# Kernel optimization log

Hardware: AMD Instinct MI355X
Metric: run time of the kernel (lower is better)

Reference implementation:

```python
import jax, jax.numpy as jnp
import numpy as np

B1, B2 = 4096, 4096
DF, MF = 1024, 512
H1, H2, H3, H1_ = 2048, 1024, 512, 1024
DO, MO = 1, 1


def _lin(x, W, b):
    return x @ W.T + b


def setup_inputs() -> dict:
    key = jax.random.key(0)
    ks = jax.random.split(key, 22)

    def w(k, o, i):
        return (jax.random.normal(k, (o, i), jnp.float32) / np.sqrt(i)).astype(jnp.float32)

    def bz(k, o):
        return jax.random.normal(k, (o,), jnp.float32) * 0.01

    return {
        'x1': jax.random.normal(ks[0], (B1, DF), jnp.float32),
        'x2': jax.random.normal(ks[1], (B2, MF), jnp.float32),
        'W1_1': w(ks[2], H1, DF),  'b1_1': bz(ks[3], H1),
        'W1_2': w(ks[4], H2, H1),  'b1_2': bz(ks[5], H2),
        'W1_3': w(ks[6], H3, H2),  'b1_3': bz(ks[7], H3),
        'W1_4': w(ks[8], H2, H3),  'b1_4': bz(ks[9], H2),
        'W1_5': w(ks[10], H1, H2), 'b1_5': bz(ks[11], H1),
        'Wp1':  w(ks[12], DO, H1), 'bp1':  bz(ks[13], DO),
        'W2_1': w(ks[14], H1_, MF), 'b2_1': bz(ks[15], H1_),
        'W2_2': w(ks[16], H3, H1_), 'b2_2': bz(ks[17], H3),
        'W2_3': w(ks[18], H1_, H3), 'b2_3': bz(ks[19], H1_),
        'Wp2':  w(ks[20], MO, H1_), 'bp2':  bz(ks[21], MO),
    }


def reference(x1, x2, W1_1, b1_1, W1_2, b1_2, W1_3, b1_3, W1_4, b1_4,
              W1_5, b1_5, Wp1, bp1, W2_1, b2_1, W2_2, b2_2, W2_3, b2_3,
              Wp2, bp2):
    # dropout: eval mode (identity)
    h = jax.nn.relu(_lin(x1, W1_1, b1_1))
    h = jax.nn.relu(_lin(h, W1_2, b1_2))
    x_1 = jax.nn.sigmoid(_lin(h, W1_3, b1_3))          # [B1, H3]
    h = jax.nn.relu(_lin(x_1, W1_4, b1_4))
    h = jax.nn.relu(_lin(h, W1_5, b1_5))
    x2_1 = jax.nn.sigmoid(_lin(h, Wp1, bp1))           # [B1, DO]

    g = jax.nn.relu(_lin(x2, W2_1, b2_1))
    x_2 = jax.nn.sigmoid(_lin(g, W2_2, b2_2))          # [B2, H3]
    g = jax.nn.relu(_lin(x_2, W2_3, b2_3))
    x2_2 = jax.nn.sigmoid(_lin(g, Wp2, bp2))           # [B2, MO]

    # Python loop over x_1 rows doing (x_2 * row).sum(1) == single GEMM x_1 @ x_2.T
    scores = x_1 @ x_2.T                                # [B1, B2]
    pre_dm = scores.reshape(-1)                         # row-major matches torch.cat order
    # MinMaxScaler.fit_transform on detached values (original uses .data -> no grad)
    pre_dm = jax.lax.stop_gradient(pre_dm)
    mn, mx = pre_dm.min(), pre_dm.max()
    pre_dm = (pre_dm - mn) / (mx - mn)

    pre_data = x2_1.reshape(-1)
    pre_model = x2_2.T.reshape(-1)
    return (pre_data, pre_dm, pre_model)
```

## Files before the change

### kernel.cpp

```cpp
#include <hip/hip_runtime.h>
#include <hip/hip_bf16.h>

typedef __bf16 bf16_t;
typedef bf16_t bf16x8 __attribute__((ext_vector_type(8)));
typedef bf16_t bf16x4 __attribute__((ext_vector_type(4)));
typedef float f32x4 __attribute__((ext_vector_type(4)));

typedef __attribute__((address_space(1))) const void gconst_void;
typedef __attribute__((address_space(3))) void lds_void;

__device__ __forceinline__ void async16(const bf16_t* g, bf16_t* l) {
  __builtin_amdgcn_global_load_lds((gconst_void*)g, (lds_void*)l, 16, 0, 0);
}

struct CvtDesc { const float* src; bf16_t* dst; long n; };
struct CvtArgs { CvtDesc d[10]; };

__global__ __launch_bounds__(256) void cvt_many(CvtArgs a) {
  const CvtDesc de = a.d[blockIdx.y];
  long i = ((long)blockIdx.x * 256 + threadIdx.x) * 4;
  const long stride = (long)gridDim.x * 256 * 4;
  for (; i < de.n; i += stride) {
    float4 v = *(const float4*)(de.src + i);
    bf16x4 o;
    o[0] = (bf16_t)v.x; o[1] = (bf16_t)v.y; o[2] = (bf16_t)v.z; o[3] = (bf16_t)v.w;
    *(bf16x4*)(de.dst + i) = o;
  }
}

struct GDesc {
  const bf16_t* A; const bf16_t* W; const float* bias; void* C;
  int N, K, act;
};
struct GArgs { GDesc d[2]; int ntiles0; };

template <typename OutT, bool MINMAX>
__global__ __launch_bounds__(256) void gemm_gb(GArgs ga, float* __restrict__ pmin,
                                               float* __restrict__ pmax) {
  const int b = blockIdx.x;
  const int p = (b >= ga.ntiles0) ? 1 : 0;
  const GDesc d = ga.d[p];
  const int local = b - (p ? ga.ntiles0 : 0);
  const int bm = (local & 31) * 128;
  const int bn = (local >> 5) * 64;
  const int N = d.N, K = d.K;

  __shared__ __align__(16) bf16_t As[2][128 * 32];
  __shared__ __align__(16) bf16_t Bs[2][64 * 32];

  const int t = threadIdx.x;
  const int wave = t >> 6;
  const int lane = t & 63;
  const int quad = lane >> 4;
  const int l15 = lane & 15;
  const int wm = (wave >> 1) * 64;
  const int wn = (wave & 1) * 32;

  f32x4 acc[4][2];
#pragma unroll
  for (int i = 0; i < 4; ++i)
#pragma unroll
    for (int j = 0; j < 2; ++j) acc[i][j] = (f32x4){0.f, 0.f, 0.f, 0.f};

  const int c0 = t, c1 = t + 256;
  const int r0 = c0 >> 2, kc0 = ((c0 & 3) - r0) & 3;
  const int r1 = c1 >> 2, kc1 = ((c1 & 3) - r1) & 3;
  const bf16_t* pa0 = d.A + (long)(bm + r0) * K + kc0 * 8;
  const bf16_t* pa1 = d.A + (long)(bm + r1) * K + kc1 * 8;
  const bf16_t* pw0 = d.W + (long)(bn + r0) * K + kc0 * 8;
  bf16_t* lA0 = &As[0][c0 * 8]; bf16_t* lA1 = &As[0][c1 * 8];
  bf16_t* lB0 = &Bs[0][c0 * 8];
  const int bufOffA = 128 * 32;
  const int bufOffB = 64 * 32;

  async16(pa0, lA0); async16(pa1, lA1);
  async16(pw0, lB0);

  int buf = 0;
  for (int k0 = 0; k0 < K; k0 += 32) {
    __syncthreads();
    const int kn = k0 + 32;
    if (kn < K) {
      const int oA = (buf ^ 1) * bufOffA;
      const int oB = (buf ^ 1) * bufOffB;
      async16(pa0 + kn, lA0 + oA); async16(pa1 + kn, lA1 + oA);
      async16(pw0 + kn, lB0 + oB);
    }
    const bf16_t* as = As[buf];
    const bf16_t* bs = Bs[buf];
    bf16x8 af[4], bfr[2];
#pragma unroll
    for (int i = 0; i < 4; ++i) {
      const int r = wm + i * 16 + l15;
      af[i] = *(const bf16x8*)&as[r * 32 + ((quad + r) & 3) * 8];
    }
#pragma unroll
    for (int j = 0; j < 2; ++j) {
      const int r = wn + j * 16 + l15;
      bfr[j] = *(const bf16x8*)&bs[r * 32 + ((quad + r) & 3) * 8];
    }
#pragma unroll
    for (int i = 0; i < 4; ++i)
#pragma unroll
      for (int j = 0; j < 2; ++j)
        acc[i][j] = __builtin_amdgcn_mfma_f32_16x16x32_bf16(bfr[j], af[i],
                                                            acc[i][j], 0, 0, 0);
    buf ^= 1;
  }

  OutT* C = (OutT*)d.C;
  const int row0 = bm + wm + l15;
  const int col0 = bn + wn + quad * 4;
  float mn = 3.4e38f, mx = -3.4e38f;
#pragma unroll
  for (int i = 0; i < 4; ++i) {
    const long row = row0 + i * 16;
#pragma unroll
    for (int j = 0; j < 2; ++j) {
      const int col = col0 + j * 16;
      f32x4 bv = d.bias ? *(const f32x4*)&d.bias[col] : (f32x4){0.f, 0.f, 0.f, 0.f};
      f32x4 v;
#pragma unroll
      for (int r = 0; r < 4; ++r) {
        float x = acc[i][j][r] + bv[r];
        if (d.act == 1) x = fmaxf(x, 0.f);
        else if (d.act == 2) x = 1.f / (1.f + expf(-x));
        v[r] = x;
        if (MINMAX) { mn = fminf(mn, x); mx = fmaxf(mx, x); }
      }
      if constexpr (sizeof(OutT) == 4) {
        *(f32x4*)&((float*)C)[row * N + col] = v;
      } else {
        bf16x4 o;
        o[0] = (bf16_t)v[0]; o[1] = (bf16_t)v[1];
        o[2] = (bf16_t)v[2]; o[3] = (bf16_t)v[3];
        *(bf16x4*)&((bf16_t*)C)[row * N + col] = o;
      }
    }
  }
  if (MINMAX) {
#pragma unroll
    for (int off = 32; off > 0; off >>= 1) {
      mn = fminf(mn, __shfl_down(mn, off));
      mx = fmaxf(mx, __shfl_down(mx, off));
    }
    __shared__ float smn[4], smx[4];
    if (lane == 0) { smn[wave] = mn; smx[wave] = mx; }
    __syncthreads();
    if (t == 0) {
      pmin[blockIdx.x] = fminf(fminf(smn[0], smn[1]), fminf(smn[2], smn[3]));
      pmax[blockIdx.x] = fmaxf(fmaxf(smx[0], smx[1]), fmaxf(smx[2], smx[3]));
    }
  }
}

struct RDesc { const bf16_t* A; const float* w; const float* b; float* out; int K; };

__global__ __launch_bounds__(64) void rowdot2(RDesc d0, RDesc d1) {
  const RDesc d = blockIdx.y ? d1 : d0;
  const int row = blockIdx.x;
  const int lane = threadIdx.x;
  const bf16_t* a = d.A + (long)row * d.K;
  float s = 0.f;
  for (int k = lane * 8; k < d.K; k += 64 * 8) {
    bf16x8 av = *(const bf16x8*)&a[k];
    float4 w0 = *(const float4*)&d.w[k];
    float4 w1 = *(const float4*)&d.w[k + 4];
    s += (float)av[0] * w0.x + (float)av[1] * w0.y +
         (float)av[2] * w0.z + (float)av[3] * w0.w +
         (float)av[4] * w1.x + (float)av[5] * w1.y +
         (float)av[6] * w1.z + (float)av[7] * w1.w;
  }
#pragma unroll
  for (int off = 32; off > 0; off >>= 1) s += __shfl_down(s, off);
  if (lane == 0) d.out[row] = 1.f / (1.f + expf(-(s + d.b[0])));
}

__global__ __launch_bounds__(256) void minmax_final(
    const float* __restrict__ pmin, const float* __restrict__ pmax, int nb,
    float* __restrict__ res) {
  float mn = 3.4e38f, mx = -3.4e38f;
  for (int i = threadIdx.x; i < nb; i += 256) {
    mn = fminf(mn, pmin[i]);
    mx = fmaxf(mx, pmax[i]);
  }
#pragma unroll
  for (int off = 32; off > 0; off >>= 1) {
    mn = fminf(mn, __shfl_down(mn, off));
    mx = fmaxf(mx, __shfl_down(mx, off));
  }
  __shared__ float smn[4], smx[4];
  const int wv = threadIdx.x >> 6, ln = threadIdx.x & 63;
  if (ln == 0) { smn[wv] = mn; smx[wv] = mx; }
  __syncthreads();
  if (threadIdx.x == 0) {
    float m0 = fminf(fminf(smn[0], smn[1]), fminf(smn[2], smn[3]));
    float m1 = fmaxf(fmaxf(smx[0], smx[1]), fmaxf(smx[2], smx[3]));
    res[0] = m0;
    res[1] = 1.f / (m1 - m0);
  }
}

__global__ __launch_bounds__(256) void normalize_k(
    float* __restrict__ out, const float* __restrict__ res, long n) {
  const float mn = res[0], inv = res[1];
  long i = ((long)blockIdx.x * 256 + threadIdx.x) * 4;
  const long stride = (long)gridDim.x * 256 * 4;
  for (; i < n; i += stride) {
    float4 v = *(const float4*)&out[i];
    v.x = (v.x - mn) * inv;
    v.y = (v.y - mn) * inv;
    v.z = (v.z - mn) * inv;
    v.w = (v.w - mn) * inv;
    *(float4*)&out[i] = v;
  }
}

extern "C" void kernel_launch(void* const* d_in, const int* in_sizes, int n_in,
                              void* d_out, int out_size, void* d_ws,
                              size_t ws_size, hipStream_t stream) {
  const float* x1   = (const float*)d_in[0];
  const float* x2   = (const float*)d_in[1];
  const float* W1_1 = (const float*)d_in[2];   const float* b1_1 = (const float*)d_in[3];
  const float* W1_2 = (const float*)d_in[4];   const float* b1_2 = (const float*)d_in[5];
  const float* W1_3 = (const float*)d_in[6];   const float* b1_3 = (const float*)d_in[7];
  const float* W1_4 = (const float*)d_in[8];   const float* b1_4 = (const float*)d_in[9];
  const float* W1_5 = (const float*)d_in[10];  const float* b1_5 = (const float*)d_in[11];
  const float* Wp1  = (const float*)d_in[12];  const float* bp1  = (const float*)d_in[13];
  const float* W2_1 = (const float*)d_in[14];  const float* b2_1 = (const float*)d_in[15];
  const float* W2_2 = (const float*)d_in[16];  const float* b2_2 = (const float*)d_in[17];
  const float* W2_3 = (const float*)d_in[18];  const float* b2_3 = (const float*)d_in[19];
  const float* Wp2  = (const float*)d_in[20];  const float* bp2  = (const float*)d_in[21];

  float* out = (float*)d_out;
  float* out_pre_data  = out;
  float* out_pre_dm    = out + 4096;
  float* out_pre_model = out + 4096 + (long)4096 * 4096;

  char* arena = (char*)out_pre_dm;
  const size_t MB = 1024 * 1024;
  bf16_t* x1b   = (bf16_t*)(arena);
  bf16_t* x2b   = (bf16_t*)(arena + 8 * MB);
  bf16_t* W1_1b = (bf16_t*)(arena + 12 * MB);
  bf16_t* W1_2b = (bf16_t*)(arena + 16 * MB);
  bf16_t* W1_3b = (bf16_t*)(arena + 20 * MB);
  bf16_t* W1_4b = (bf16_t*)(arena + 21 * MB);
  bf16_t* W1_5b = (bf16_t*)(arena + 22 * MB);
  bf16_t* W2_1b = (bf16_t*)(arena + 26 * MB);
  bf16_t* W2_2b = (bf16_t*)(arena + 27 * MB);
  bf16_t* W2_3b = (bf16_t*)(arena + 28 * MB);
  bf16_t* bufA  = (bf16_t*)(arena + 32 * MB);
  bf16_t* bufB  = (bf16_t*)(arena + 48 * MB);
  bf16_t* bufC  = (bf16_t*)(arena + 56 * MB);

  char* ws = (char*)d_ws;
  bf16_t* bufX1 = (bf16_t*)(ws);
  bf16_t* bufX2 = (bf16_t*)(ws + 4 * MB);
  float* pmin = (float*)(ws + 8 * MB);
  float* pmax = pmin + 2048;
  float* res  = pmax + 2048;

  CvtArgs ca;
  ca.d[0] = {x1,   x1b,   (long)4096 * 1024};
  ca.d[1] = {x2,   x2b,   (long)4096 * 512};
  ca.d[2] = {W1_1, W1_1b, (long)2048 * 1024};
  ca.d[3] = {W1_2, W1_2b, (long)1024 * 2048};
  ca.d[4] = {W1_3, W1_3b, (long)512 * 1024};
  ca.d[5] = {W1_4, W1_4b, (long)1024 * 512};
  ca.d[6] = {W1_5, W1_5b, (long)2048 * 1024};
  ca.d[7] = {W2_1, W2_1b, (long)1024 * 512};
  ca.d[8] = {W2_2, W2_2b, (long)512 * 1024};
  ca.d[9] = {W2_3, W2_3b, (long)1024 * 512};
  cvt_many<<<dim3(192, 10), 256, 0, stream>>>(ca);

  const long nS = (long)4096 * 4096;
  GArgs g;

  g.d[0] = {x1b, W1_1b, b1_1, bufA, 2048, 1024, 1};
  g.d[1] = {x2b, W2_1b, b2_1, bufC, 1024, 512, 1};
  g.ntiles0 = 1024;
  gemm_gb<bf16_t, false><<<1536, 256, 0, stream>>>(g, nullptr, nullptr);

  g.d[0] = {bufA, W1_2b, b1_2, bufB, 1024, 2048, 1};
  g.d[1] = {bufC, W2_2b, b2_2, bufX2, 512, 1024, 2};
  g.ntiles0 = 512;
  gemm_gb<bf16_t, false><<<768, 256, 0, stream>>>(g, nullptr, nullptr);

  g.d[0] = {bufB, W1_3b, b1_3, bufX1, 512, 1024, 2};
  g.d[1] = {bufX2, W2_3b, b2_3, bufC, 1024, 512, 1};
  g.ntiles0 = 256;
  gemm_gb<bf16_t, false><<<768, 256, 0, stream>>>(g, nullptr, nullptr);

  g.d[0] = {bufX1, W1_4b, b1_4, bufB, 1024, 512, 1};
  g.d[1] = g.d[0];
  g.ntiles0 = 512;
  gemm_gb<bf16_t, false><<<512, 256, 0, stream>>>(g, nullptr, nullptr);

  g.d[0] = {bufB, W1_5b, b1_5, bufA, 2048, 1024, 1};
  g.d[1] = g.d[0];
  g.ntiles0 = 1024;
  gemm_gb<bf16_t, false><<<1024, 256, 0, stream>>>(g, nullptr, nullptr);

  RDesc r0 = {bufA, Wp1, bp1, out_pre_data, 2048};
  RDesc r1 = {bufC, Wp2, bp2, out_pre_model, 1024};
  rowdot2<<<dim3(4096, 2), 64, 0, stream>>>(r0, r1);

  g.d[0] = {bufX1, bufX2, nullptr, out_pre_dm, 4096, 512, 0};
  g.d[1] = g.d[0];
  g.ntiles0 = 2048;
  gemm_gb<float, true><<<2048, 256, 0, stream>>>(g, pmin, pmax);

  minmax_final<<<1, 256, 0, stream>>>(pmin, pmax, 2048, res);
  normalize_k<<<2048, 256, 0, stream>>>(out_pre_dm, res, nS);
}
```

Before: 359.1 us.

## Load GEMM weight fragments directly into registers, bypassing LDS, and adjust A swizzle

The weight (B) tile is no longer staged through shared memory. Each wave loads its own 16-row B fragments straight from global memory into registers, one k-step ahead, which removes the B LDS traffic and the B LDS reads. The A-tile swizzle also changes to spread LDS bank conflicts. The cost is that B is no longer shared between the two wave rows, so global and L2 traffic for weights doubles. The uncoalesced per-lane 16-byte loads also add register pressure and latency exposure.

```diff
diff --git a/kernel.cpp b/kernel.cpp
--- a/kernel.cpp
+++ b/kernel.cpp
@@ -46,7 +46,6 @@
   const int N = d.N, K = d.K;
 
   __shared__ __align__(16) bf16_t As[2][128 * 32];
-  __shared__ __align__(16) bf16_t Bs[2][64 * 32];
 
   const int t = threadIdx.x;
   const int wave = t >> 6;
@@ -63,48 +62,46 @@
     for (int j = 0; j < 2; ++j) acc[i][j] = (f32x4){0.f, 0.f, 0.f, 0.f};
 
   const int c0 = t, c1 = t + 256;
-  const int r0 = c0 >> 2, kc0 = ((c0 & 3) - r0) & 3;
-  const int r1 = c1 >> 2, kc1 = ((c1 & 3) - r1) & 3;
+  const int r0 = c0 >> 2, kc0 = ((c0 & 3) - r0 - (r0 >> 2)) & 3;
+  const int r1 = c1 >> 2, kc1 = ((c1 & 3) - r1 - (r1 >> 2)) & 3;
   const bf16_t* pa0 = d.A + (long)(bm + r0) * K + kc0 * 8;
   const bf16_t* pa1 = d.A + (long)(bm + r1) * K + kc1 * 8;
-  const bf16_t* pw0 = d.W + (long)(bn + r0) * K + kc0 * 8;
   bf16_t* lA0 = &As[0][c0 * 8]; bf16_t* lA1 = &As[0][c1 * 8];
-  bf16_t* lB0 = &Bs[0][c0 * 8];
   const int bufOffA = 128 * 32;
-  const int bufOffB = 64 * 32;
+
+  const bf16_t* pB0 = d.W + (long)(bn + wn + l15) * K + quad * 8;
+  const bf16_t* pB1 = pB0 + (long)16 * K;
 
   async16(pa0, lA0); async16(pa1, lA1);
-  async16(pw0, lB0);
+  bf16x8 bcur0 = *(const bf16x8*)pB0;
+  bf16x8 bcur1 = *(const bf16x8*)pB1;
 
   int buf = 0;
   for (int k0 = 0; k0 < K; k0 += 32) {
     __syncthreads();
     const int kn = k0 + 32;
+    bf16x8 bnext0, bnext1;
     if (kn < K) {
       const int oA = (buf ^ 1) * bufOffA;
-      const int oB = (buf ^ 1) * bufOffB;
       async16(pa0 + kn, lA0 + oA); async16(pa1 + kn, lA1 + oA);
-      async16(pw0 + kn, lB0 + oB);
+      bnext0 = *(const bf16x8*)(pB0 + kn);
+      bnext1 = *(const bf16x8*)(pB1 + kn);
     }
     const bf16_t* as = As[buf];
-    const bf16_t* bs = Bs[buf];
-    bf16x8 af[4], bfr[2];
+    bf16x8 af[4];
 #pragma unroll
     for (int i = 0; i < 4; ++i) {
       const int r = wm + i * 16 + l15;
-      af[i] = *(const bf16x8*)&as[r * 32 + ((quad + r) & 3) * 8];
-    }
-#pragma unroll
-    for (int j = 0; j < 2; ++j) {
-      const int r = wn + j * 16 + l15;
-      bfr[j] = *(const bf16x8*)&bs[r * 32 + ((quad + r) & 3) * 8];
-    }
-#pragma unroll
-    for (int i = 0; i < 4; ++i)
-#pragma unroll
-      for (int j = 0; j < 2; ++j)
-        acc[i][j] = __builtin_amdgcn_mfma_f32_16x16x32_bf16(bfr[j], af[i],
-                                                            acc[i][j], 0, 0, 0);
+      af[i] = *(const bf16x8*)&as[r * 32 + ((quad + r + (r >> 2)) & 3) * 8];
+    }
+#pragma unroll
+    for (int i = 0; i < 4; ++i) {
+      acc[i][0] = __builtin_amdgcn_mfma_f32_16x16x32_bf16(bcur0, af[i],
+                                                          acc[i][0], 0, 0, 0);
+      acc[i][1] = __builtin_amdgcn_mfma_f32_16x16x32_bf16(bcur1, af[i],
+                                                          acc[i][1], 0, 0, 0);
+    }
+    bcur0 = bnext0; bcur1 = bnext1;
     buf ^= 1;
   }
 
```

Result: slower. 424.0 us (+18.1%).
